# Kernel optimization log

Measured on AMD Instinct MI355X. Metric: run time of the kernel, lower is better.

## Reference

```python
import jax, jax.numpy as jnp
import numpy as np

N_SLICES = 2  # init kwarg n_slices


def affine_grid_3d(theta, D, H, W):
    """torch.nn.functional.affine_grid for 5D output, align_corners=False.
    theta: [B,3,4]; returns grid [B,D,H,W,3] with last dim (x,y,z) ~ (W,H,D)."""
    xs = (jnp.arange(W, dtype=theta.dtype) + 0.5) * (2.0 / W) - 1.0
    ys = (jnp.arange(H, dtype=theta.dtype) + 0.5) * (2.0 / H) - 1.0
    zs = (jnp.arange(D, dtype=theta.dtype) + 0.5) * (2.0 / D) - 1.0
    zz, yy, xx = jnp.meshgrid(zs, ys, xs, indexing='ij')
    base = jnp.stack([xx, yy, zz, jnp.ones_like(xx)], axis=-1)  # [D,H,W,4]
    return jnp.einsum('bij,dhwj->bdhwi', theta, base)  # [B,D,H,W,3]


def grid_sample_3d_zeros(vol, grid):
    """torch.nn.functional.grid_sample, mode='bilinear' (trilinear for 5D),
    padding_mode='zeros', align_corners=False.
    vol: [B,C,D,H,W]; grid: [B,D,H,W,3] normalized xyz coords."""
    B, C, D, H, W = vol.shape
    ix = ((grid[..., 0] + 1.0) * W - 1.0) * 0.5
    iy = ((grid[..., 1] + 1.0) * H - 1.0) * 0.5
    iz = ((grid[..., 2] + 1.0) * D - 1.0) * 0.5
    ix0 = jnp.floor(ix); iy0 = jnp.floor(iy); iz0 = jnp.floor(iz)
    fx = ix - ix0; fy = iy - iy0; fz = iz - iz0

    def gather(v, z, y, x):  # v: [C,D,H,W], idx: [D,H,W] -> [C,D,H,W]
        return v[:, z, y, x]

    out = jnp.zeros((B, C, D, H, W), vol.dtype)
    for dz in (0, 1):
        for dy in (0, 1):
            for dx in (0, 1):
                xi = ix0 + dx; yi = iy0 + dy; zi = iz0 + dz
                w = (jnp.where(dx, fx, 1.0 - fx)
                     * jnp.where(dy, fy, 1.0 - fy)
                     * jnp.where(dz, fz, 1.0 - fz))
                valid = ((xi >= 0) & (xi < W) & (yi >= 0) & (yi < H)
                         & (zi >= 0) & (zi < D))
                xc = jnp.clip(xi, 0, W - 1).astype(jnp.int32)
                yc = jnp.clip(yi, 0, H - 1).astype(jnp.int32)
                zc = jnp.clip(zi, 0, D - 1).astype(jnp.int32)
                vals = jax.vmap(gather)(vol, zc, yc, xc)  # [B,C,D,H,W]
                out = out + vals * (w * valid)[:, None]
    return out


def skip_connector(x, b_grid_affines):
    B, C, SPAT, _ = x.shape
    # zero volume with the 2D slice stack placed at the central W-plane
    vol = jnp.zeros((B, C, SPAT, SPAT, SPAT), x.dtype).at[..., SPAT // 2].set(x)
    chunks = jnp.split(vol, N_SLICES, axis=1)
    outs = []
    for i in range(N_SLICES):
        aff = b_grid_affines[i].astype(jnp.float32)  # [B,4,4]
        # get_zooms: column norms of rotation block
        zooms = jnp.sqrt((aff[:, :3, :3] ** 2).sum(axis=1))  # [B,3]
        # rescale_rot_components_with_diag(aff, 1/zooms) == aff @ diag(1/zx,1/zy,1/zz,1)
        scale = jnp.concatenate([1.0 / zooms, jnp.ones((aff.shape[0], 1), aff.dtype)], axis=1)
        aff = aff * scale[:, None, :]
        theta = jnp.linalg.inv(aff)[:, :3, :]  # [B,3,4]
        grid = affine_grid_3d(theta, SPAT, SPAT, SPAT)
        outs.append(grid_sample_3d_zeros(chunks[i], grid))
    return jnp.concatenate(outs, axis=1)  # [B,C,SPAT,SPAT,SPAT]


def setup_inputs() -> dict:
    key = jax.random.key(0)
    k1, k2 = jax.random.split(key)
    B, C, SPAT = 2, 32, 96
    x = jax.random.normal(k1, (B, C, SPAT, SPAT), dtype=jnp.float32)
    # near-identity invertible homogeneous affines for the two views (SA, HLA)
    noise = 0.1 * jax.random.normal(k2, (2, B, 4, 4), dtype=jnp.float32)
    aff = jnp.eye(4, dtype=jnp.float32)[None, None] + noise
    aff = aff.at[..., 3, :].set(jnp.array([0.0, 0.0, 0.0, 1.0], dtype=jnp.float32))
    return {"x": x, "b_grid_affines": aff}


def reference(x, b_grid_affines):
    return skip_connector(x, b_grid_affines)
```

## Files before the change

kernel.cpp:

```cpp
#include <hip/hip_runtime.h>
#include <math.h>

#define SPAT 96
#define PLANE (SPAT*SPAT*SPAT)
#define IMG   (SPAT*SPAT)
#define OUT_FLOATS (64 * PLANE)

__device__ inline void invert4(const float m[16], float inv[16]) {
    inv[0]  =  m[5]*m[10]*m[15] - m[5]*m[11]*m[14] - m[9]*m[6]*m[15] + m[9]*m[7]*m[14] + m[13]*m[6]*m[11] - m[13]*m[7]*m[10];
    inv[4]  = -m[4]*m[10]*m[15] + m[4]*m[11]*m[14] + m[8]*m[6]*m[15] - m[8]*m[7]*m[14] - m[12]*m[6]*m[11] + m[12]*m[7]*m[10];
    inv[8]  =  m[4]*m[9]*m[15]  - m[4]*m[11]*m[13] - m[8]*m[5]*m[15] + m[8]*m[7]*m[13] + m[12]*m[5]*m[11] - m[12]*m[7]*m[9];
    inv[12] = -m[4]*m[9]*m[14]  + m[4]*m[10]*m[13] + m[8]*m[5]*m[14] - m[8]*m[6]*m[13] - m[12]*m[5]*m[10] + m[12]*m[6]*m[9];
    inv[1]  = -m[1]*m[10]*m[15] + m[1]*m[11]*m[14] + m[9]*m[2]*m[15] - m[9]*m[3]*m[14] - m[13]*m[2]*m[11] + m[13]*m[3]*m[10];
    inv[5]  =  m[0]*m[10]*m[15] - m[0]*m[11]*m[14] - m[8]*m[2]*m[15] + m[8]*m[3]*m[14] + m[12]*m[2]*m[11] - m[12]*m[3]*m[10];
    inv[9]  = -m[0]*m[9]*m[15]  + m[0]*m[11]*m[13] + m[8]*m[1]*m[15] - m[8]*m[3]*m[13] - m[12]*m[1]*m[11] + m[12]*m[3]*m[9];
    inv[13] =  m[0]*m[9]*m[14]  - m[0]*m[10]*m[13] - m[8]*m[1]*m[14] + m[8]*m[2]*m[13] + m[12]*m[1]*m[10] - m[12]*m[2]*m[9];
    inv[2]  =  m[1]*m[6]*m[15]  - m[1]*m[7]*m[14]  - m[5]*m[2]*m[15] + m[5]*m[3]*m[14] + m[13]*m[2]*m[7]  - m[13]*m[3]*m[6];
    inv[6]  = -m[0]*m[6]*m[15]  + m[0]*m[7]*m[14]  + m[4]*m[2]*m[15] - m[4]*m[3]*m[14] - m[12]*m[2]*m[7]  + m[12]*m[3]*m[6];
    inv[10] =  m[0]*m[5]*m[15]  - m[0]*m[7]*m[13]  - m[4]*m[1]*m[15] + m[4]*m[3]*m[13] + m[12]*m[1]*m[7]  - m[12]*m[3]*m[5];
    inv[14] = -m[0]*m[5]*m[14]  + m[0]*m[6]*m[13]  + m[4]*m[1]*m[14] - m[4]*m[2]*m[13] - m[12]*m[1]*m[6]  + m[12]*m[2]*m[5];
    inv[3]  = -m[1]*m[6]*m[11]  + m[1]*m[7]*m[10]  + m[5]*m[2]*m[11] - m[5]*m[3]*m[10] - m[9]*m[2]*m[7]   + m[9]*m[3]*m[6];
    inv[7]  =  m[0]*m[6]*m[11]  - m[0]*m[7]*m[10]  - m[4]*m[2]*m[11] + m[4]*m[3]*m[10] + m[8]*m[2]*m[7]   - m[8]*m[3]*m[6];
    inv[11] = -m[0]*m[5]*m[11]  + m[0]*m[7]*m[9]   + m[4]*m[1]*m[11] - m[4]*m[3]*m[9]  - m[8]*m[1]*m[7]   + m[8]*m[3]*m[5];
    inv[15] =  m[0]*m[5]*m[10]  - m[0]*m[6]*m[9]   - m[4]*m[1]*m[10] + m[4]*m[2]*m[9]  + m[8]*m[1]*m[6]   - m[8]*m[2]*m[5];
    float det  = m[0]*inv[0] + m[1]*inv[4] + m[2]*inv[8] + m[3]*inv[12];
    float rdet = 1.0f / det;
    for (int i = 0; i < 16; ++i) inv[i] *= rdet;
}

__global__ __launch_bounds__(256) void zero_kernel(float4* __restrict__ out) {
    const size_t n4 = OUT_FLOATS / 4;
    size_t i = (size_t)blockIdx.x * 256 + threadIdx.x;
    size_t stride = (size_t)gridDim.x * 256;
    float4 z = make_float4(0.f, 0.f, 0.f, 0.f);
    for (; i < n4; i += stride) out[i] = z;
}

__global__ __launch_bounds__(256) void slab_kernel(
        const float* __restrict__ xin,
        const float* __restrict__ aff_in,
        float* __restrict__ out) {
    __shared__ float Ms[12];
    int sb = blockIdx.y;
    if (threadIdx.x == 0) {
        float A[16];
        #pragma unroll
        for (int i = 0; i < 16; ++i) A[i] = aff_in[sb * 16 + i];
        #pragma unroll
        for (int j = 0; j < 3; ++j) {
            float z = sqrtf(A[0*4+j]*A[0*4+j] + A[1*4+j]*A[1*4+j] + A[2*4+j]*A[2*4+j]);
            float rz = 1.0f / z;
            #pragma unroll
            for (int i = 0; i < 4; ++i) A[i*4+j] *= rz;
        }
        float inv[16];
        invert4(A, inv);
        #pragma unroll
        for (int r = 0; r < 3; ++r) {
            float T0 = inv[r*4+0], T1 = inv[r*4+1], T2 = inv[r*4+2], T3 = inv[r*4+3];
            Ms[r*4+0] = T0;
            Ms[r*4+1] = T1;
            Ms[r*4+2] = T2;
            Ms[r*4+3] = -47.5f * (T0 + T1 + T2) + 48.0f * T3 + 47.5f;
        }
    }
    __syncthreads();

    int t    = blockIdx.x * 256 + threadIdx.x;
    int cg   = t & 3;
    int qpar = (t >> 2) & 1;
    int hd   = t >> 3;
    int h    = hd % SPAT;
    int d    = hd / SPAT;
    int s    = sb >> 1;
    int b    = sb & 1;

    float Mxw = Ms[0], Mxh = Ms[1], Mxd = Ms[2],  Mx0 = Ms[3];
    float Myw = Ms[4], Myh = Ms[5], Myd = Ms[6],  My0 = Ms[7];
    float Mzw = Ms[8], Mzh = Ms[9], Mzd = Ms[10], Mz0 = Ms[11];

    float fh = (float)h, fd = (float)d;
    float bx = Mxh * fh + Mxd * fd + Mx0;

    int wlo, whi;
    if (fabsf(Mxw) > 1e-6f) {
        float rMxw = 1.0f / Mxw;
        float w1 = (47.0f - bx) * rMxw;
        float w2 = (49.0f - bx) * rMxw;
        float wmin = fminf(w1, w2), wmax = fmaxf(w1, w2);
        wlo = max((int)ceilf(wmin), 0);
        whi = min((int)floorf(wmax), SPAT - 1);
    } else {
        bool in = fabsf(bx - 48.0f) < 1.0f;
        wlo = in ? 0 : 1;
        whi = in ? SPAT - 1 : 0;
    }
    if (wlo > whi) return;
    int qlo = (wlo >> 2) + qpar, qhi = whi >> 2;

    float by = Myh * fh + Myd * fd + My0;
    float bz = Mzh * fh + Mzd * fd + Mz0;

    size_t cbase = (size_t)(b * 32 + s * 16 + cg * 4);
    const float* img = xin + cbase * (size_t)IMG;
    float* op = out + cbase * (size_t)PLANE + ((size_t)d * SPAT + h) * SPAT;

    for (int q = qlo; q <= qhi; q += 2) {
        float v[4][4];
        #pragma unroll
        for (int j = 0; j < 4; ++j) {
            float fw = (float)(4 * q + j);
            float ix = Mxw * fw + bx;
            float wx = 1.0f - fabsf(ix - 48.0f);
            if (wx > 0.0f) {
                float iy = Myw * fw + by;
                float iz = Mzw * fw + bz;
                float yf = floorf(iy), zf = floorf(iz);
                float fy = iy - yf,    fz = iz - zf;
                int y0 = (int)yf, z0 = (int)zf;
                bool vy0 = (y0 >= 0)  & (y0 <  SPAT);
                bool vy1 = (y0 >= -1) & (y0 <  SPAT - 1);
                bool vz0 = (z0 >= 0)  & (z0 <  SPAT);
                bool vz1 = (z0 >= -1) & (z0 <  SPAT - 1);
                int y0c = min(max(y0, 0),     SPAT - 1);
                int y1c = min(max(y0 + 1, 0), SPAT - 1);
                int z0c = min(max(z0, 0),     SPAT - 1);
                int z1c = min(max(z0 + 1, 0), SPAT - 1);
                float wy0 = 1.0f - fy, wy1 = fy;
                float wz0 = 1.0f - fz, wz1 = fz;
                float w00 = wx * wz0 * wy0 * ((vz0 & vy0) ? 1.0f : 0.0f);
                float w01 = wx * wz0 * wy1 * ((vz0 & vy1) ? 1.0f : 0.0f);
                float w10 = wx * wz1 * wy0 * ((vz1 & vy0) ? 1.0f : 0.0f);
                float w11 = wx * wz1 * wy1 * ((vz1 & vy1) ? 1.0f : 0.0f);
                int o00 = z0c * SPAT + y0c, o01 = z0c * SPAT + y1c;
                int o10 = z1c * SPAT + y0c, o11 = z1c * SPAT + y1c;
                #pragma unroll
                for (int c = 0; c < 4; ++c) {
                    const float* ic = img + (size_t)c * IMG;
                    v[c][j] = w00 * ic[o00] + w01 * ic[o01]
                            + w10 * ic[o10] + w11 * ic[o11];
                }
            } else {
                #pragma unroll
                for (int c = 0; c < 4; ++c) v[c][j] = 0.0f;
            }
        }
        #pragma unroll
        for (int c = 0; c < 4; ++c) {
            *reinterpret_cast<float4*>(op + (size_t)c * PLANE + 4 * q) =
                make_float4(v[c][0], v[c][1], v[c][2], v[c][3]);
        }
    }
}

extern "C" void kernel_launch(void* const* d_in, const int* in_sizes, int n_in,
                              void* d_out, int out_size, void* d_ws, size_t ws_size,
                              hipStream_t stream) {
    const float* x   = (const float*)d_in[0];
    const float* aff = (const float*)d_in[1];
    float* out = (float*)d_out;

    zero_kernel<<<4096, 256, 0, stream>>>((float4*)out);

    dim3 grid(288, 4);
    slab_kernel<<<grid, 256, 0, stream>>>(x, aff, out);
}
```

Before: 235.5 us.

## Fuse output zeroing into sampling kernel with one block per depth-channel plane

Removes the separate zero-fill kernel and has a single kernel write every output float4, storing zeros or sampled values per W-quad. Each block covers one (depth, channel) plane of 96x96 in 9 coalesced iterations, and a per-quad x-range test skips sampling for quads far from the central plane. This avoids writing the output twice and drops one launch. The cost is that the four-channel reuse of computed coordinates and weights is lost, since each thread now handles a single channel.

```diff
diff --git a/kernel.cpp b/kernel.cpp
--- a/kernel.cpp
+++ b/kernel.cpp
@@ -1,10 +1,10 @@
 #include <hip/hip_runtime.h>
 #include <math.h>
 
-#define SPAT 96
+#define SPAT  96
+#define IMG   (SPAT*SPAT)
 #define PLANE (SPAT*SPAT*SPAT)
-#define IMG   (SPAT*SPAT)
-#define OUT_FLOATS (64 * PLANE)
+#define ROWCH (IMG/4)
 
 __device__ inline void invert4(const float m[16], float inv[16]) {
     inv[0]  =  m[5]*m[10]*m[15] - m[5]*m[11]*m[14] - m[9]*m[6]*m[15] + m[9]*m[7]*m[14] + m[13]*m[6]*m[11] - m[13]*m[7]*m[10];
@@ -28,20 +28,17 @@
     for (int i = 0; i < 16; ++i) inv[i] *= rdet;
 }
 
-__global__ __launch_bounds__(256) void zero_kernel(float4* __restrict__ out) {
-    const size_t n4 = OUT_FLOATS / 4;
-    size_t i = (size_t)blockIdx.x * 256 + threadIdx.x;
-    size_t stride = (size_t)gridDim.x * 256;
-    float4 z = make_float4(0.f, 0.f, 0.f, 0.f);
-    for (; i < n4; i += stride) out[i] = z;
-}
-
-__global__ __launch_bounds__(256) void slab_kernel(
+__global__ __launch_bounds__(256) void fused_kernel(
         const float* __restrict__ xin,
         const float* __restrict__ aff_in,
-        float* __restrict__ out) {
+        float4* __restrict__ out) {
     __shared__ float Ms[12];
-    int sb = blockIdx.y;
+    const int d  = blockIdx.x;
+    const int cc = blockIdx.y;
+    const int b  = cc >> 5;
+    const int s  = (cc >> 4) & 1;
+    const int sb = s * 2 + b;
+
     if (threadIdx.x == 0) {
         float A[16];
         #pragma unroll
@@ -66,90 +63,68 @@
     }
     __syncthreads();
 
-    int t    = blockIdx.x * 256 + threadIdx.x;
-    int cg   = t & 3;
-    int qpar = (t >> 2) & 1;
-    int hd   = t >> 3;
-    int h    = hd % SPAT;
-    int d    = hd / SPAT;
-    int s    = sb >> 1;
-    int b    = sb & 1;
+    const float Mxw = Ms[0], Mxh = Ms[1], Mxd = Ms[2],  Mx0 = Ms[3];
+    const float Myw = Ms[4], Myh = Ms[5], Myd = Ms[6],  My0 = Ms[7];
+    const float Mzw = Ms[8], Mzh = Ms[9], Mzd = Ms[10], Mz0 = Ms[11];
 
-    float Mxw = Ms[0], Mxh = Ms[1], Mxd = Ms[2],  Mx0 = Ms[3];
-    float Myw = Ms[4], Myh = Ms[5], Myd = Ms[6],  My0 = Ms[7];
-    float Mzw = Ms[8], Mzh = Ms[9], Mzd = Ms[10], Mz0 = Ms[11];
+    const float fd   = (float)d;
+    const float bx_d = Mxd * fd + Mx0;
+    const float by_d = Myd * fd + My0;
+    const float bz_d = Mzd * fd + Mz0;
 
-    float fh = (float)h, fd = (float)d;
-    float bx = Mxh * fh + Mxd * fd + Mx0;
+    const float* img = xin + (size_t)cc * IMG;
+    float4* op = out + ((size_t)cc * (PLANE / 4) + (size_t)d * (IMG / 4));
 
-    int wlo, whi;
-    if (fabsf(Mxw) > 1e-6f) {
-        float rMxw = 1.0f / Mxw;
-        float w1 = (47.0f - bx) * rMxw;
-        float w2 = (49.0f - bx) * rMxw;
-        float wmin = fminf(w1, w2), wmax = fmaxf(w1, w2);
-        wlo = max((int)ceilf(wmin), 0);
-        whi = min((int)floorf(wmax), SPAT - 1);
-    } else {
-        bool in = fabsf(bx - 48.0f) < 1.0f;
-        wlo = in ? 0 : 1;
-        whi = in ? SPAT - 1 : 0;
-    }
-    if (wlo > whi) return;
-    int qlo = (wlo >> 2) + qpar, qhi = whi >> 2;
+    #pragma unroll 3
+    for (int it = 0; it < 9; ++it) {
+        int tl = (int)threadIdx.x + 256 * it;
+        int h  = tl / 24;
+        int w4 = tl - h * 24;
+        float fh  = (float)h;
+        float bx  = Mxh * fh + bx_d;
+        float fw0 = (float)(w4 << 2);
+        float ix0 = Mxw * fw0 + bx;
+        float ix3 = ix0 + 3.0f * Mxw;
 
-    float by = Myh * fh + Myd * fd + My0;
-    float bz = Mzh * fh + Mzd * fd + Mz0;
-
-    size_t cbase = (size_t)(b * 32 + s * 16 + cg * 4);
-    const float* img = xin + cbase * (size_t)IMG;
-    float* op = out + cbase * (size_t)PLANE + ((size_t)d * SPAT + h) * SPAT;
-
-    for (int q = qlo; q <= qhi; q += 2) {
-        float v[4][4];
-        #pragma unroll
-        for (int j = 0; j < 4; ++j) {
-            float fw = (float)(4 * q + j);
-            float ix = Mxw * fw + bx;
-            float wx = 1.0f - fabsf(ix - 48.0f);
-            if (wx > 0.0f) {
-                float iy = Myw * fw + by;
-                float iz = Mzw * fw + bz;
-                float yf = floorf(iy), zf = floorf(iz);
-                float fy = iy - yf,    fz = iz - zf;
-                int y0 = (int)yf, z0 = (int)zf;
-                bool vy0 = (y0 >= 0)  & (y0 <  SPAT);
-                bool vy1 = (y0 >= -1) & (y0 <  SPAT - 1);
-                bool vz0 = (z0 >= 0)  & (z0 <  SPAT);
-                bool vz1 = (z0 >= -1) & (z0 <  SPAT - 1);
-                int y0c = min(max(y0, 0),     SPAT - 1);
-                int y1c = min(max(y0 + 1, 0), SPAT - 1);
-                int z0c = min(max(z0, 0),     SPAT - 1);
-                int z1c = min(max(z0 + 1, 0), SPAT - 1);
-                float wy0 = 1.0f - fy, wy1 = fy;
-                float wz0 = 1.0f - fz, wz1 = fz;
-                float w00 = wx * wz0 * wy0 * ((vz0 & vy0) ? 1.0f : 0.0f);
-                float w01 = wx * wz0 * wy1 * ((vz0 & vy1) ? 1.0f : 0.0f);
-                float w10 = wx * wz1 * wy0 * ((vz1 & vy0) ? 1.0f : 0.0f);
-                float w11 = wx * wz1 * wy1 * ((vz1 & vy1) ? 1.0f : 0.0f);
-                int o00 = z0c * SPAT + y0c, o01 = z0c * SPAT + y1c;
-                int o10 = z1c * SPAT + y0c, o11 = z1c * SPAT + y1c;
-                #pragma unroll
-                for (int c = 0; c < 4; ++c) {
-                    const float* ic = img + (size_t)c * IMG;
-                    v[c][j] = w00 * ic[o00] + w01 * ic[o01]
-                            + w10 * ic[o10] + w11 * ic[o11];
+        float4 v = make_float4(0.f, 0.f, 0.f, 0.f);
+        if (fmaxf(ix0, ix3) > 47.0f && fminf(ix0, ix3) < 49.0f) {
+            float by = Myh * fh + by_d;
+            float bz = Mzh * fh + bz_d;
+            float vv[4];
+            #pragma unroll
+            for (int j = 0; j < 4; ++j) {
+                float fw = fw0 + (float)j;
+                float ix = Mxw * fw + bx;
+                float wx = 1.0f - fabsf(ix - 48.0f);
+                float r = 0.0f;
+                if (wx > 0.0f) {
+                    float iy = Myw * fw + by;
+                    float iz = Mzw * fw + bz;
+                    float yf = floorf(iy), zf = floorf(iz);
+                    float fy = iy - yf,    fz = iz - zf;
+                    int y0 = (int)yf, z0 = (int)zf;
+                    bool vy0 = (y0 >= 0)  & (y0 <  SPAT);
+                    bool vy1 = (y0 >= -1) & (y0 <  SPAT - 1);
+                    bool vz0 = (z0 >= 0)  & (z0 <  SPAT);
+                    bool vz1 = (z0 >= -1) & (z0 <  SPAT - 1);
+                    int y0c = min(max(y0, 0),     SPAT - 1);
+                    int y1c = min(max(y0 + 1, 0), SPAT - 1);
+                    int z0c = min(max(z0, 0),     SPAT - 1);
+                    int z1c = min(max(z0 + 1, 0), SPAT - 1);
+                    float wy0 = 1.0f - fy, wy1 = fy;
+                    float wz0 = 1.0f - fz, wz1 = fz;
+                    float w00 = wx * wz0 * wy0 * ((vz0 & vy0) ? 1.0f : 0.0f);
+                    float w01 = wx * wz0 * wy1 * ((vz0 & vy1) ? 1.0f : 0.0f);
+                    float w10 = wx * wz1 * wy0 * ((vz1 & vy0) ? 1.0f : 0.0f);
+                    float w11 = wx * wz1 * wy1 * ((vz1 & vy1) ? 1.0f : 0.0f);
+                    r = w00 * img[z0c * SPAT + y0c] + w01 * img[z0c * SPAT + y1c]
+                      + w10 * img[z1c * SPAT + y0c] + w11 * img[z1c * SPAT + y1c];
                 }
-            } else {
-                #pragma unroll
-                for (int c = 0; c < 4; ++c) v[c][j] = 0.0f;
+                vv[j] = r;
             }
+            v = make_float4(vv[0], vv[1], vv[2], vv[3]);
         }
-        #pragma unroll
-        for (int c = 0; c < 4; ++c) {
-            *reinterpret_cast<float4*>(op + (size_t)c * PLANE + 4 * q) =
-                make_float4(v[c][0], v[c][1], v[c][2], v[c][3]);
-        }
+        op[tl] = v;
     }
 }
 
@@ -160,8 +135,6 @@
     const float* aff = (const float*)d_in[1];
     float* out = (float*)d_out;
 
-    zero_kernel<<<4096, 256, 0, stream>>>((float4*)out);
-
-    dim3 grid(288, 4);
-    slab_kernel<<<grid, 256, 0, stream>>>(x, aff, out);
+    dim3 grid(SPAT, 64);
+    fused_kernel<<<grid, 256, 0, stream>>>(x, aff, (float4*)out);
 }
```

Result: slower. 250.4 us (+6.3%).
